# Performance work log

Hardware: AMD Instinct MI355X
Metric: run time of the kernel (lower is better)

The kernel has to match this reference:

```python
import jax, jax.numpy as jnp
import numpy as np

N = 100_000          # nodes
E = 1_600_000        # real edges (self-loops appended after)
HID = 32             # hidden_dim
RES = 5              # PersistenceImager resolution -> 5x5 image
SIGMA = 0.2          # gaussian bandwidth of persistence image kernel
PRELU_A = 0.1        # F.prelu weight used in the source


def _linear_init(k, fan_in, fan_out):
    k1, k2 = jax.random.split(k)
    s = 1.0 / np.sqrt(fan_in)
    W = jax.random.uniform(k1, (fan_in, fan_out), minval=-s, maxval=s, dtype=jnp.float32)
    b = jax.random.uniform(k2, (fan_out,), minval=-s, maxval=s, dtype=jnp.float32)
    return W, b


def setup_inputs() -> dict:
    key = jax.random.key(0)
    ks = jax.random.split(key, 10)
    # edge list: E random edges, then N self-loops appended at the END
    src = jax.random.randint(ks[0], (E,), 0, N)
    dst = jax.random.randint(ks[1], (E,), 0, N)
    loops = jnp.arange(N)
    edge_index0 = jnp.stack([jnp.concatenate([src, loops]),
                             jnp.concatenate([dst, loops])]).astype(jnp.int64)
    x0 = jax.random.normal(ks[2], (N, 1), dtype=jnp.float32)
    # GIN conv MLPs (Base_Model with out_dim=hidden_dim)
    W1, b1 = _linear_init(ks[3], 1, HID)
    W2, b2 = _linear_init(ks[4], HID, HID)
    W4, b4 = _linear_init(ks[5], HID, HID)
    W3, b3 = _linear_init(ks[6], HID, HID)   # conv3: Linear only, no ReLU
    W5, b5 = _linear_init(ks[7], 2 * HID, HID)  # lin5
    W6, b6 = _linear_init(ks[8], HID, 2)        # lin6
    return dict(x0=x0, edge_index0=edge_index0,
                W1=W1, b1=b1, W2=W2, b2=b2, W4=W4, b4=b4, W3=W3, b3=b3,
                W5=W5, b5=b5, W6=W6, b6=b6)


def _gin_agg(x, src, dst):
    # PyG GINConv with eps=0: (1+eps)*x + sum_{j->i} x_j  (aggregation over the
    # provided edge_index, which here already includes appended self-loops)
    return x + jax.ops.segment_sum(x[src], dst, num_segments=N)


def _prelu(x):
    return jnp.where(x >= 0, x, PRELU_A * x)


def _pers_image(pd):
    # Persistence image on a RESxRES grid over [0,1]^2 of (birth, persistence),
    # gaussian kernel integrated per pixel via normal CDFs, linear pers weight.
    b = pd[:, 0]
    pers = pd[:, 1] - pd[:, 0]
    edges = jnp.linspace(0.0, 1.0, RES + 1)
    inv = 1.0 / (SIGMA * np.sqrt(2.0))
    cdf_b = 0.5 * (1.0 + jax.lax.erf((edges[None, :] - b[:, None]) * inv))   # [E, RES+1]
    cdf_p = 0.5 * (1.0 + jax.lax.erf((edges[None, :] - pers[:, None]) * inv))
    db = cdf_b[:, 1:] - cdf_b[:, :-1]   # [E, RES]
    dp = cdf_p[:, 1:] - cdf_p[:, :-1]
    img = jnp.einsum('e,ei,ej->ij', pers, db, dp)
    return img.reshape(-1)  # [25]


def reference(x0, edge_index0, W1, b1, W2, b2, W4, b4, W3, b3, W5, b5, W6, b6):
    src, dst = edge_index0[0], edge_index0[1]
    # Base_Model GIN path (dropout is identity in eval mode); order 1,2,4,3
    x = jax.nn.relu(_gin_agg(x0, src, dst) @ W1 + b1)
    x = jax.nn.relu(_gin_agg(x, src, dst) @ W2 + b2)
    x = jax.nn.relu(_gin_agg(x, src, dst) @ W4 + b4)
    x = _gin_agg(x, src, dst) @ W3 + b3      # conv3: Linear, no ReLU
    # edge head over the E real edges (drop trailing N self-loops)
    x_in = x[src[:E]]
    x_out = x[dst[:E]]
    h = _prelu(jnp.concatenate([x_in, x_out], axis=-1) @ W5 + b5)
    pd = h @ W6 + b6                          # predicted PD, [E, 2]
    img = _pers_image(pd)                     # persistence image, [25]
    return pd, img
```

## Files before the change

### kernel.cpp

```cpp
#include <hip/hip_runtime.h>
#include <hip/hip_bf16.h>
#include <hip/hip_fp16.h>
#include <math.h>

#define NN 100000
#define EE 1600000
#define ET 1700000
#define HID 32

#define BKT_SHIFT 10
#define BKT_MASK 1023
#define NBKT 98
#define EPB 4096
#define NBLK_A 416

__global__ __launch_bounds__(128) void k_zero(int* __restrict__ p, int n) {
    int t = blockIdx.x * 128 + threadIdx.x;
    if (t < n) p[t] = 0;
}

__global__ __launch_bounds__(256) void k_bkt_count(const int* __restrict__ dst32, int* __restrict__ bucket_cnt) {
    __shared__ int h[NBKT];
    for (int i = threadIdx.x; i < NBKT; i += 256) h[i] = 0;
    __syncthreads();
    int base = blockIdx.x * EPB;
    for (int k = 0; k < EPB; k += 256) {
        int t = base + k + threadIdx.x;
        if (t < ET) atomicAdd(&h[dst32[t] >> BKT_SHIFT], 1);
    }
    __syncthreads();
    for (int i = threadIdx.x; i < NBKT; i += 256) {
        int c = h[i];
        if (c) atomicAdd(&bucket_cnt[i], c);
    }
}

__global__ __launch_bounds__(128) void k_bkt_scan(const int* __restrict__ bucket_cnt, int* __restrict__ bucket_base,
                                                  int* __restrict__ bucket_fill) {
    __shared__ int s[128];
    int t = threadIdx.x;
    int v = (t < NBKT) ? bucket_cnt[t] : 0;
    s[t] = v;
    for (int off = 1; off < 128; off <<= 1) {
        __syncthreads();
        int u = (t >= off) ? s[t - off] : 0;
        __syncthreads();
        s[t] += u;
    }
    __syncthreads();
    int ex = s[t] - v;
    if (t < NBKT) {
        bucket_base[t] = ex;
        bucket_fill[t] = ex;
    }
    if (t == 0) bucket_base[NBKT] = ET;
}

__global__ __launch_bounds__(256) void k_bkt_scatter(const int* __restrict__ src32, const int* __restrict__ dst32,
                                                     int* __restrict__ bucket_fill, int2* __restrict__ pairs) {
    __shared__ int h[NBKT];
    __shared__ int bbase[NBKT];
    for (int i = threadIdx.x; i < NBKT; i += 256) h[i] = 0;
    __syncthreads();
    int base = blockIdx.x * EPB;
    for (int k = 0; k < EPB; k += 256) {
        int t = base + k + threadIdx.x;
        if (t < ET) atomicAdd(&h[dst32[t] >> BKT_SHIFT], 1);
    }
    __syncthreads();
    for (int i = threadIdx.x; i < NBKT; i += 256) {
        int c = h[i];
        bbase[i] = c ? atomicAdd(&bucket_fill[i], c) : 0;
        h[i] = 0;
    }
    __syncthreads();
    for (int k = 0; k < EPB; k += 256) {
        int t = base + k + threadIdx.x;
        if (t < ET) {
            int sv = src32[t], dv = dst32[t];
            int b = dv >> BKT_SHIFT;
            int off = atomicAdd(&h[b], 1);
            pairs[bbase[b] + off] = make_int2(sv, dv);
        }
    }
}

__global__ __launch_bounds__(512) void k_bkt_csr(const int2* __restrict__ pairs, const int* __restrict__ bucket_base,
                                                 int* __restrict__ rowptr, int* __restrict__ src_sorted) {
    __shared__ int h[1024];
    __shared__ int tmp[512];
    int t = threadIdx.x;
    int b = blockIdx.x;
    int e0 = bucket_base[b], e1 = bucket_base[b + 1];
    int node0 = b << BKT_SHIFT;

    h[t] = 0;
    h[t + 512] = 0;
    __syncthreads();
    for (int e = e0 + t; e < e1; e += 512) atomicAdd(&h[pairs[e].y & BKT_MASK], 1);
    __syncthreads();

    int i0 = 2 * t, i1 = 2 * t + 1;
    int v0 = h[i0], v1 = h[i1];
    int s = v0 + v1;
    tmp[t] = s;
    for (int off = 1; off < 512; off <<= 1) {
        __syncthreads();
        int u = (t >= off) ? tmp[t - off] : 0;
        __syncthreads();
        tmp[t] += u;
    }
    __syncthreads();
    int excl = tmp[t] - s;
    h[i0] = excl;
    h[i1] = excl + v0;
    __syncthreads();

    for (int i = t; i < 1024; i += 512) {
        int node = node0 + i;
        if (node < NN) rowptr[node] = e0 + h[i];
    }
    if (b == 0 && t == 0) rowptr[NN] = ET;
    __syncthreads();

    for (int e = e0 + t; e < e1; e += 512) {
        int2 p = pairs[e];
        int sl = atomicAdd(&h[p.y & BKT_MASK], 1);
        src_sorted[e0 + sl] = p.x;
    }
}

__device__ __forceinline__ void acc4(uint2 r, float& c0, float& c1, float& c2, float& c3) {
    __half2 h0 = *reinterpret_cast<__half2*>(&r.x);
    __half2 h1 = *reinterpret_cast<__half2*>(&r.y);
    float2 f0 = __half22float2(h0);
    float2 f1 = __half22float2(h1);
    c0 += f0.x; c1 += f0.y; c2 += f1.x; c3 += f1.y;
}

__global__ __launch_bounds__(256) void k_pull1a(const int* __restrict__ rowptr, const int* __restrict__ src_sorted,
                                                const float* __restrict__ x0, float* __restrict__ agg0) {
    int g = blockIdx.x * 256 + threadIdx.x;
    if (g >= NN) return;
    int e0 = rowptr[g], e1 = rowptr[g + 1];
    float a0 = x0[g], a1 = 0.f, a2 = 0.f, a3 = 0.f, a4 = 0.f, a5 = 0.f, a6 = 0.f, a7 = 0.f;
    int e = e0;
    for (; e + 8 <= e1; e += 8) {
        a0 += x0[src_sorted[e + 0]];
        a1 += x0[src_sorted[e + 1]];
        a2 += x0[src_sorted[e + 2]];
        a3 += x0[src_sorted[e + 3]];
        a4 += x0[src_sorted[e + 4]];
        a5 += x0[src_sorted[e + 5]];
        a6 += x0[src_sorted[e + 6]];
        a7 += x0[src_sorted[e + 7]];
    }
    for (; e < e1; ++e) a0 += x0[src_sorted[e]];
    agg0[g] = ((a0 + a1) + (a2 + a3)) + ((a4 + a5) + (a6 + a7));
}

__global__ __launch_bounds__(256) void k_pull1b(const float* __restrict__ agg0, const float* __restrict__ W1,
                                                const float* __restrict__ b1, __half* __restrict__ hout) {
    int t = blockIdx.x * 256 + threadIdx.x;
    int g = t >> 3, j = t & 7;
    float s = agg0[g];
    float o0 = fmaxf(fmaf(s, W1[4 * j + 0], b1[4 * j + 0]), 0.f);
    float o1 = fmaxf(fmaf(s, W1[4 * j + 1], b1[4 * j + 1]), 0.f);
    float o2 = fmaxf(fmaf(s, W1[4 * j + 2], b1[4 * j + 2]), 0.f);
    float o3 = fmaxf(fmaf(s, W1[4 * j + 3], b1[4 * j + 3]), 0.f);
    __half2 p0 = __floats2half2_rn(o0, o1);
    __half2 p1 = __floats2half2_rn(o2, o3);
    uint2 st = make_uint2(*reinterpret_cast<unsigned*>(&p0), *reinterpret_cast<unsigned*>(&p1));
    reinterpret_cast<uint2*>(hout)[(g << 3) + j] = st;
}

template <int RELU>
__global__ __launch_bounds__(256) void k_agg_mm(const int* __restrict__ rowptr, const int* __restrict__ src_sorted,
                                                const __half* __restrict__ hin, const float* __restrict__ W,
                                                const float* __restrict__ b, __half* __restrict__ hout) {
    __shared__ float Wl[1024];
    for (int i = threadIdx.x; i < 1024; i += 256) Wl[i] = W[i];
    __syncthreads();
    int g = (blockIdx.x * 256 + threadIdx.x) >> 3;
    int j = threadIdx.x & 7;
    const uint2* tab = reinterpret_cast<const uint2*>(hin);
    int e0 = rowptr[g], e1 = rowptr[g + 1];
    float x0, x1, x2, x3;
    {
        uint2 r = tab[(g << 3) + j];
        __half2 h0 = *reinterpret_cast<__half2*>(&r.x);
        __half2 h1 = *reinterpret_cast<__half2*>(&r.y);
        float2 f0 = __half22float2(h0), f1 = __half22float2(h1);
        x0 = f0.x; x1 = f0.y; x2 = f1.x; x3 = f1.y;
    }
    float y0 = 0.f, y1 = 0.f, y2 = 0.f, y3 = 0.f;
    int e = e0;
    for (; e + 8 <= e1; e += 8) {
        int s0 = src_sorted[e + 0], s1 = src_sorted[e + 1], s2 = src_sorted[e + 2], s3 = src_sorted[e + 3];
        int s4 = src_sorted[e + 4], s5 = src_sorted[e + 5], s6 = src_sorted[e + 6], s7 = src_sorted[e + 7];
        uint2 r0 = tab[(s0 << 3) + j];
        uint2 r1 = tab[(s1 << 3) + j];
        uint2 r2 = tab[(s2 << 3) + j];
        uint2 r3 = tab[(s3 << 3) + j];
        uint2 r4 = tab[(s4 << 3) + j];
        uint2 r5 = tab[(s5 << 3) + j];
        uint2 r6 = tab[(s6 << 3) + j];
        uint2 r7 = tab[(s7 << 3) + j];
        acc4(r0, x0, x1, x2, x3);
        acc4(r1, y0, y1, y2, y3);
        acc4(r2, x0, x1, x2, x3);
        acc4(r3, y0, y1, y2, y3);
        acc4(r4, x0, x1, x2, x3);
        acc4(r5, y0, y1, y2, y3);
        acc4(r6, x0, x1, x2, x3);
        acc4(r7, y0, y1, y2, y3);
    }
    for (; e < e1; ++e) {
        uint2 r = tab[(src_sorted[e] << 3) + j];
        acc4(r, x0, x1, x2, x3);
    }
    x0 += y0; x1 += y1; x2 += y2; x3 += y3;

    float o0 = b[4 * j + 0], o1 = b[4 * j + 1], o2 = b[4 * j + 2], o3 = b[4 * j + 3];
#pragma unroll
    for (int k = 0; k < 8; ++k) {
        float f0 = __shfl(x0, k, 8);
        float f1 = __shfl(x1, k, 8);
        float f2 = __shfl(x2, k, 8);
        float f3 = __shfl(x3, k, 8);
        float4 w0 = *reinterpret_cast<const float4*>(&Wl[(4 * k + 0) * 32 + 4 * j]);
        float4 w1 = *reinterpret_cast<const float4*>(&Wl[(4 * k + 1) * 32 + 4 * j]);
        float4 w2 = *reinterpret_cast<const float4*>(&Wl[(4 * k + 2) * 32 + 4 * j]);
        float4 w3 = *reinterpret_cast<const float4*>(&Wl[(4 * k + 3) * 32 + 4 * j]);
        o0 = fmaf(f0, w0.x, o0); o1 = fmaf(f0, w0.y, o1); o2 = fmaf(f0, w0.z, o2); o3 = fmaf(f0, w0.w, o3);
        o0 = fmaf(f1, w1.x, o0); o1 = fmaf(f1, w1.y, o1); o2 = fmaf(f1, w1.z, o2); o3 = fmaf(f1, w1.w, o3);
        o0 = fmaf(f2, w2.x, o0); o1 = fmaf(f2, w2.y, o1); o2 = fmaf(f2, w2.z, o2); o3 = fmaf(f2, w2.w, o3);
        o0 = fmaf(f3, w3.x, o0); o1 = fmaf(f3, w3.y, o1); o2 = fmaf(f3, w3.z, o2); o3 = fmaf(f3, w3.w, o3);
    }
    if (RELU) {
        o0 = fmaxf(o0, 0.f); o1 = fmaxf(o1, 0.f); o2 = fmaxf(o2, 0.f); o3 = fmaxf(o3, 0.f);
    }
    __half2 p0 = __floats2half2_rn(o0, o1);
    __half2 p1 = __floats2half2_rn(o2, o3);
    uint2 st = make_uint2(*reinterpret_cast<unsigned*>(&p0), *reinterpret_cast<unsigned*>(&p1));
    reinterpret_cast<uint2*>(hout)[(g << 3) + j] = st;
}

__global__ __launch_bounds__(256) void k_agg_mm_proj(const int* __restrict__ rowptr, const int* __restrict__ src_sorted,
                                                     const __half* __restrict__ hin, const float* __restrict__ W3,
                                                     const float* __restrict__ b3,
                                                     const float* __restrict__ W5, const float* __restrict__ b5,
                                                     __half* __restrict__ u16, __half* __restrict__ v16) {
    __shared__ float W3l[1024];
    __shared__ float W5l[2048];
    for (int i = threadIdx.x; i < 1024; i += 256) W3l[i] = W3[i];
    for (int i = threadIdx.x; i < 2048; i += 256) W5l[i] = W5[i];
    __syncthreads();
    int g = (blockIdx.x * 256 + threadIdx.x) >> 3;
    int j = threadIdx.x & 7;
    const uint2* tab = reinterpret_cast<const uint2*>(hin);
    int e0 = rowptr[g], e1 = rowptr[g + 1];
    float x0, x1, x2, x3;
    {
        uint2 r = tab[(g << 3) + j];
        __half2 h0 = *reinterpret_cast<__half2*>(&r.x);
        __half2 h1 = *reinterpret_cast<__half2*>(&r.y);
        float2 f0 = __half22float2(h0), f1 = __half22float2(h1);
        x0 = f0.x; x1 = f0.y; x2 = f1.x; x3 = f1.y;
    }
    float y0 = 0.f, y1 = 0.f, y2 = 0.f, y3 = 0.f;
    int e = e0;
    for (; e + 8 <= e1; e += 8) {
        int s0 = src_sorted[e + 0], s1 = src_sorted[e + 1], s2 = src_sorted[e + 2], s3 = src_sorted[e + 3];
        int s4 = src_sorted[e + 4], s5 = src_sorted[e + 5], s6 = src_sorted[e + 6], s7 = src_sorted[e + 7];
        uint2 r0 = tab[(s0 << 3) + j];
        uint2 r1 = tab[(s1 << 3) + j];
        uint2 r2 = tab[(s2 << 3) + j];
        uint2 r3 = tab[(s3 << 3) + j];
        uint2 r4 = tab[(s4 << 3) + j];
        uint2 r5 = tab[(s5 << 3) + j];
        uint2 r6 = tab[(s6 << 3) + j];
        uint2 r7 = tab[(s7 << 3) + j];
        acc4(r0, x0, x1, x2, x3);
        acc4(r1, y0, y1, y2, y3);
        acc4(r2, x0, x1, x2, x3);
        acc4(r3, y0, y1, y2, y3);
        acc4(r4, x0, x1, x2, x3);
        acc4(r5, y0, y1, y2, y3);
        acc4(r6, x0, x1, x2, x3);
        acc4(r7, y0, y1, y2, y3);
    }
    for (; e < e1; ++e) {
        uint2 r = tab[(src_sorted[e] << 3) + j];
        acc4(r, x0, x1, x2, x3);
    }
    x0 += y0; x1 += y1; x2 += y2; x3 += y3;

    float o0 = b3[4 * j + 0], o1 = b3[4 * j + 1], o2 = b3[4 * j + 2], o3 = b3[4 * j + 3];
#pragma unroll
    for (int k = 0; k < 8; ++k) {
        float f0 = __shfl(x0, k, 8);
        float f1 = __shfl(x1, k, 8);
        float f2 = __shfl(x2, k, 8);
        float f3 = __shfl(x3, k, 8);
        float4 w0 = *reinterpret_cast<const float4*>(&W3l[(4 * k + 0) * 32 + 4 * j]);
        float4 w1 = *reinterpret_cast<const float4*>(&W3l[(4 * k + 1) * 32 + 4 * j]);
        float4 w2 = *reinterpret_cast<const float4*>(&W3l[(4 * k + 2) * 32 + 4 * j]);
        float4 w3 = *reinterpret_cast<const float4*>(&W3l[(4 * k + 3) * 32 + 4 * j]);
        o0 = fmaf(f0, w0.x, o0); o1 = fmaf(f0, w0.y, o1); o2 = fmaf(f0, w0.z, o2); o3 = fmaf(f0, w0.w, o3);
        o0 = fmaf(f1, w1.x, o0); o1 = fmaf(f1, w1.y, o1); o2 = fmaf(f1, w1.z, o2); o3 = fmaf(f1, w1.w, o3);
        o0 = fmaf(f2, w2.x, o0); o1 = fmaf(f2, w2.y, o1); o2 = fmaf(f2, w2.z, o2); o3 = fmaf(f2, w2.w, o3);
        o0 = fmaf(f3, w3.x, o0); o1 = fmaf(f3, w3.y, o1); o2 = fmaf(f3, w3.z, o2); o3 = fmaf(f3, w3.w, o3);
    }
    float u0 = b5[4 * j + 0], u1 = b5[4 * j + 1], u2 = b5[4 * j + 2], u3 = b5[4 * j + 3];
    float v0 = 0.f, v1 = 0.f, v2 = 0.f, v3 = 0.f;
#pragma unroll
    for (int k = 0; k < 8; ++k) {
        float f0 = __shfl(o0, k, 8);
        float f1 = __shfl(o1, k, 8);
        float f2 = __shfl(o2, k, 8);
        float f3 = __shfl(o3, k, 8);
        float4 a0 = *reinterpret_cast<const float4*>(&W5l[(4 * k + 0) * 32 + 4 * j]);
        float4 a1 = *reinterpret_cast<const float4*>(&W5l[(4 * k + 1) * 32 + 4 * j]);
        float4 a2 = *reinterpret_cast<const float4*>(&W5l[(4 * k + 2) * 32 + 4 * j]);
        float4 a3 = *reinterpret_cast<const float4*>(&W5l[(4 * k + 3) * 32 + 4 * j]);
        u0 = fmaf(f0, a0.x, u0); u1 = fmaf(f0, a0.y, u1); u2 = fmaf(f0, a0.z, u2); u3 = fmaf(f0, a0.w, u3);
        u0 = fmaf(f1, a1.x, u0); u1 = fmaf(f1, a1.y, u1); u2 = fmaf(f1, a1.z, u2); u3 = fmaf(f1, a1.w, u3);
        u0 = fmaf(f2, a2.x, u0); u1 = fmaf(f2, a2.y, u1); u2 = fmaf(f2, a2.z, u2); u3 = fmaf(f2, a2.w, u3);
        u0 = fmaf(f3, a3.x, u0); u1 = fmaf(f3, a3.y, u1); u2 = fmaf(f3, a3.z, u2); u3 = fmaf(f3, a3.w, u3);
        float4 c0 = *reinterpret_cast<const float4*>(&W5l[(32 + 4 * k + 0) * 32 + 4 * j]);
        float4 c1 = *reinterpret_cast<const float4*>(&W5l[(32 + 4 * k + 1) * 32 + 4 * j]);
        float4 c2 = *reinterpret_cast<const float4*>(&W5l[(32 + 4 * k + 2) * 32 + 4 * j]);
        float4 c3 = *reinterpret_cast<const float4*>(&W5l[(32 + 4 * k + 3) * 32 + 4 * j]);
        v0 = fmaf(f0, c0.x, v0); v1 = fmaf(f0, c0.y, v1); v2 = fmaf(f0, c0.z, v2); v3 = fmaf(f0, c0.w, v3);
        v0 = fmaf(f1, c1.x, v0); v1 = fmaf(f1, c1.y, v1); v2 = fmaf(f1, c1.z, v2); v3 = fmaf(f1, c1.w, v3);
        v0 = fmaf(f2, c2.x, v0); v1 = fmaf(f2, c2.y, v1); v2 = fmaf(f2, c2.z, v2); v3 = fmaf(f2, c2.w, v3);
        v0 = fmaf(f3, c3.x, v0); v1 = fmaf(f3, c3.y, v1); v2 = fmaf(f3, c3.z, v2); v3 = fmaf(f3, c3.w, v3);
    }
    __half2 pu0 = __floats2half2_rn(u0, u1);
    __half2 pu1 = __floats2half2_rn(u2, u3);
    uint2 su = make_uint2(*reinterpret_cast<unsigned*>(&pu0), *reinterpret_cast<unsigned*>(&pu1));
    reinterpret_cast<uint2*>(u16)[(g << 3) + j] = su;
    __half2 pv0 = __floats2half2_rn(v0, v1);
    __half2 pv1 = __floats2half2_rn(v2, v3);
    uint2 sv = make_uint2(*reinterpret_cast<unsigned*>(&pv0), *reinterpret_cast<unsigned*>(&pv1));
    reinterpret_cast<uint2*>(v16)[(g << 3) + j] = sv;
}

__device__ __forceinline__ void edge_pd(const uint4* pu, const uint4* pv, const float* W6,
                                        float b60, float b61, float& pd0, float& pd1) {
    pd0 = b60; pd1 = b61;
#pragma unroll
    for (int q = 0; q < 4; ++q) {
        uint4 ua = pu[q];
        uint4 vb = pv[q];
        const __half2* ah = reinterpret_cast<const __half2*>(&ua);
        const __half2* bh = reinterpret_cast<const __half2*>(&vb);
#pragma unroll
        for (int r = 0; r < 4; ++r) {
            float2 f = __half22float2(__hadd2(ah[r], bh[r]));
            int jj = q * 8 + 2 * r;
            float h0 = f.x >= 0.f ? f.x : 0.1f * f.x;
            float h1 = f.y >= 0.f ? f.y : 0.1f * f.y;
            pd0 = fmaf(h0, W6[2 * jj + 0], pd0);
            pd1 = fmaf(h0, W6[2 * jj + 1], pd1);
            pd0 = fmaf(h1, W6[2 * (jj + 1) + 0], pd0);
            pd1 = fmaf(h1, W6[2 * (jj + 1) + 1], pd1);
        }
    }
}

__global__ __launch_bounds__(256) void k_edge(const int* __restrict__ src32, const int* __restrict__ dst32,
                                              const __half* __restrict__ u16, const __half* __restrict__ v16,
                                              const float* __restrict__ W6, const float* __restrict__ b6,
                                              float* __restrict__ pd_out, float* __restrict__ partial) {
    int ea = blockIdx.x * 512 + threadIdx.x;
    int eb = ea + 256;
    int sa = src32[ea], da = dst32[ea];
    int sb = src32[eb], db = dst32[eb];
    const uint4* pua = reinterpret_cast<const uint4*>(u16 + ((size_t)sa << 5));
    const uint4* pva = reinterpret_cast<const uint4*>(v16 + ((size_t)da << 5));
    const uint4* pub = reinterpret_cast<const uint4*>(u16 + ((size_t)sb << 5));
    const uint4* pvb = reinterpret_cast<const uint4*>(v16 + ((size_t)db << 5));
    float b60 = b6[0], b61 = b6[1];

    float pda0, pda1, pdb0, pdb1;
    edge_pd(pua, pva, W6, b60, b61, pda0, pda1);
    edge_pd(pub, pvb, W6, b60, b61, pdb0, pdb1);
    reinterpret_cast<float2*>(pd_out)[ea] = make_float2(pda0, pda1);
    reinterpret_cast<float2*>(pd_out)[eb] = make_float2(pdb0, pdb1);

    float persA = pda1 - pda0;
    float persB = pdb1 - pdb0;
    const float inv = 3.5355339059327378f;
    float cbA[6], cpA[6], cbB[6], cpB[6];
#pragma unroll
    for (int i = 0; i < 6; ++i) {
        float te = 0.2f * (float)i;
        cbA[i] = 0.5f * (1.f + erff((te - pda0) * inv));
        cpA[i] = 0.5f * (1.f + erff((te - persA) * inv));
        cbB[i] = 0.5f * (1.f + erff((te - pdb0) * inv));
        cpB[i] = 0.5f * (1.f + erff((te - persB) * inv));
    }

    int lane = threadIdx.x & 63;
    int wv = threadIdx.x >> 6;
    __shared__ float sacc[4][25];
#pragma unroll
    for (int i = 0; i < 5; ++i) {
#pragma unroll
        for (int jj = 0; jj < 5; ++jj) {
            float v = persA * (cbA[i + 1] - cbA[i]) * (cpA[jj + 1] - cpA[jj])
                    + persB * (cbB[i + 1] - cbB[i]) * (cpB[jj + 1] - cpB[jj]);
            v += __shfl_down(v, 32);
            v += __shfl_down(v, 16);
            v += __shfl_down(v, 8);
            v += __shfl_down(v, 4);
            v += __shfl_down(v, 2);
            v += __shfl_down(v, 1);
            if (lane == 0) sacc[wv][i * 5 + jj] = v;
        }
    }
    __syncthreads();
    if (threadIdx.x < 25) {
        partial[(size_t)blockIdx.x * 25 + threadIdx.x] =
            sacc[0][threadIdx.x] + sacc[1][threadIdx.x] + sacc[2][threadIdx.x] + sacc[3][threadIdx.x];
    }
}

__global__ __launch_bounds__(256) void k_img(const float* __restrict__ partial, float* __restrict__ img) {
    int bin = blockIdx.x;
    float s = 0.f;
    for (int k = threadIdx.x; k < EE / 512; k += 256) s += partial[(size_t)k * 25 + bin];
    s += __shfl_down(s, 32);
    s += __shfl_down(s, 16);
    s += __shfl_down(s, 8);
    s += __shfl_down(s, 4);
    s += __shfl_down(s, 2);
    s += __shfl_down(s, 1);
    __shared__ float wsum[4];
    if ((threadIdx.x & 63) == 0) wsum[threadIdx.x >> 6] = s;
    __syncthreads();
    if (threadIdx.x == 0) img[bin] = wsum[0] + wsum[1] + wsum[2] + wsum[3];
}

extern "C" void kernel_launch(void* const* d_in, const int* in_sizes, int n_in,
                              void* d_out, int out_size, void* d_ws, size_t ws_size,
                              hipStream_t stream) {
    const float* x0 = (const float*)d_in[0];
    const int* src32 = (const int*)d_in[1];
    const int* dst32 = src32 + ET;
    const float* W1 = (const float*)d_in[2];
    const float* b1 = (const float*)d_in[3];
    const float* W2 = (const float*)d_in[4];
    const float* b2 = (const float*)d_in[5];
    const float* W4 = (const float*)d_in[6];
    const float* b4 = (const float*)d_in[7];
    const float* W3 = (const float*)d_in[8];
    const float* b3 = (const float*)d_in[9];
    const float* W5 = (const float*)d_in[10];
    const float* b5 = (const float*)d_in[11];
    const float* W6 = (const float*)d_in[12];
    const float* b6 = (const float*)d_in[13];
    float* out = (float*)d_out;

    char* w = (char*)d_ws;
    int2* pairs = (int2*)w;
    int* bucket_cnt = (int*)(pairs + ET);
    int* bucket_base = bucket_cnt + NBKT;
    int* bucket_fill = bucket_base + NBKT + 1;
    int* rowptr = bucket_fill + NBKT;
    int* src_sorted = rowptr + NN + 1;
    size_t off = ((size_t)((char*)(src_sorted + ET) - w) + 63) & ~(size_t)63;
    __half* bufA = (__half*)(w + off);
    __half* bufB = bufA + (size_t)NN * 32;
    __half* u16 = bufB + (size_t)NN * 32;
    __half* v16 = u16 + (size_t)NN * 32;
    float* agg0 = (float*)(v16 + (size_t)NN * 32);
    float* partial = agg0 + NN;

    k_zero<<<1, 128, 0, stream>>>(bucket_cnt, NBKT);
    k_bkt_count<<<NBLK_A, 256, 0, stream>>>(dst32, bucket_cnt);
    k_bkt_scan<<<1, 128, 0, stream>>>(bucket_cnt, bucket_base, bucket_fill);
    k_bkt_scatter<<<NBLK_A, 256, 0, stream>>>(src32, dst32, bucket_fill, pairs);
    k_bkt_csr<<<NBKT, 512, 0, stream>>>(pairs, bucket_base, rowptr, src_sorted);

    k_pull1a<<<(NN + 255) / 256, 256, 0, stream>>>(rowptr, src_sorted, x0, agg0);
    k_pull1b<<<NN * 8 / 256, 256, 0, stream>>>(agg0, W1, b1, bufA);
    k_agg_mm<1><<<NN * 8 / 256, 256, 0, stream>>>(rowptr, src_sorted, bufA, W2, b2, bufB);
    k_agg_mm<1><<<NN * 8 / 256, 256, 0, stream>>>(rowptr, src_sorted, bufB, W4, b4, bufA);
    k_agg_mm_proj<<<NN * 8 / 256, 256, 0, stream>>>(rowptr, src_sorted, bufA, W3, b3, W5, b5, u16, v16);

    k_edge<<<EE / 512, 256, 0, stream>>>(src32, dst32, u16, v16, W6, b6, out, partial);
    k_img<<<25, 256, 0, stream>>>(partial, out + 2 * (size_t)EE);
}
```

Baseline: 254.3 us.

## Process edges in dst-bucketed order with grid-stride loop and register image accumulation

The bucket scatter now also records each edge's original id. The edge head then walks the dst-bucketed pair list, so gathers of v16 rows hit nearby nodes and get better cache locality. Each thread accumulates the 25 image bins in registers across a grid-stride loop and reduces once per block, instead of doing a wave reduction for every pair of edges. It also folds the 0.5 CDF constants into a single 0.25 factor. The costs are scattered pd writes indexed by the original edge id, an extra index array written in the scatter, a self-loop filter branch, and higher register pressure from the 25 accumulators.

```diff
diff --git a/kernel.cpp b/kernel.cpp
--- a/kernel.cpp
+++ b/kernel.cpp
@@ -13,6 +13,7 @@
 #define NBKT 98
 #define EPB 4096
 #define NBLK_A 416
+#define NBE 1024
 
 __global__ __launch_bounds__(128) void k_zero(int* __restrict__ p, int n) {
     int t = blockIdx.x * 128 + threadIdx.x;
@@ -57,7 +58,8 @@
 }
 
 __global__ __launch_bounds__(256) void k_bkt_scatter(const int* __restrict__ src32, const int* __restrict__ dst32,
-                                                     int* __restrict__ bucket_fill, int2* __restrict__ pairs) {
+                                                     int* __restrict__ bucket_fill, int2* __restrict__ pairs,
+                                                     int* __restrict__ eidA) {
     __shared__ int h[NBKT];
     __shared__ int bbase[NBKT];
     for (int i = threadIdx.x; i < NBKT; i += 256) h[i] = 0;
@@ -80,7 +82,9 @@
             int sv = src32[t], dv = dst32[t];
             int b = dv >> BKT_SHIFT;
             int off = atomicAdd(&h[b], 1);
-            pairs[bbase[b] + off] = make_int2(sv, dv);
+            int slot = bbase[b] + off;
+            pairs[slot] = make_int2(sv, dv);
+            eidA[slot] = t;
         }
     }
 }
@@ -347,79 +351,76 @@
     reinterpret_cast<uint2*>(v16)[(g << 3) + j] = sv;
 }
 
-__device__ __forceinline__ void edge_pd(const uint4* pu, const uint4* pv, const float* W6,
-                                        float b60, float b61, float& pd0, float& pd1) {
-    pd0 = b60; pd1 = b61;
-#pragma unroll
-    for (int q = 0; q < 4; ++q) {
-        uint4 ua = pu[q];
-        uint4 vb = pv[q];
-        const __half2* ah = reinterpret_cast<const __half2*>(&ua);
-        const __half2* bh = reinterpret_cast<const __half2*>(&vb);
-#pragma unroll
-        for (int r = 0; r < 4; ++r) {
-            float2 f = __half22float2(__hadd2(ah[r], bh[r]));
-            int jj = q * 8 + 2 * r;
-            float h0 = f.x >= 0.f ? f.x : 0.1f * f.x;
-            float h1 = f.y >= 0.f ? f.y : 0.1f * f.y;
-            pd0 = fmaf(h0, W6[2 * jj + 0], pd0);
-            pd1 = fmaf(h0, W6[2 * jj + 1], pd1);
-            pd0 = fmaf(h1, W6[2 * (jj + 1) + 0], pd0);
-            pd1 = fmaf(h1, W6[2 * (jj + 1) + 1], pd1);
+__global__ __launch_bounds__(256) void k_edge2(const int2* __restrict__ pairs, const int* __restrict__ eidA,
+                                               const __half* __restrict__ u16, const __half* __restrict__ v16,
+                                               const float* __restrict__ W6, const float* __restrict__ b6,
+                                               float* __restrict__ pd_out, float* __restrict__ partial) {
+    float acc[25];
+#pragma unroll
+    for (int i = 0; i < 25; ++i) acc[i] = 0.f;
+    float b60 = b6[0], b61 = b6[1];
+    const float inv = 3.5355339059327378f;
+
+    int t0 = blockIdx.x * 256 + threadIdx.x;
+    const int stride = NBE * 256;
+    for (int e = t0; e < ET; e += stride) {
+        int2 p = pairs[e];
+        int eid = eidA[e];
+        if (eid < EE) {
+            const uint4* pu = reinterpret_cast<const uint4*>(u16 + ((size_t)p.x << 5));
+            const uint4* pv = reinterpret_cast<const uint4*>(v16 + ((size_t)p.y << 5));
+            float pd0 = b60, pd1 = b61;
+#pragma unroll
+            for (int q = 0; q < 4; ++q) {
+                uint4 ua = pu[q];
+                uint4 vb = pv[q];
+                const __half2* ah = reinterpret_cast<const __half2*>(&ua);
+                const __half2* bh = reinterpret_cast<const __half2*>(&vb);
+#pragma unroll
+                for (int r = 0; r < 4; ++r) {
+                    float2 f = __half22float2(__hadd2(ah[r], bh[r]));
+                    int jj = q * 8 + 2 * r;
+                    float h0 = f.x >= 0.f ? f.x : 0.1f * f.x;
+                    float h1 = f.y >= 0.f ? f.y : 0.1f * f.y;
+                    pd0 = fmaf(h0, W6[2 * jj + 0], pd0);
+                    pd1 = fmaf(h0, W6[2 * jj + 1], pd1);
+                    pd0 = fmaf(h1, W6[2 * (jj + 1) + 0], pd0);
+                    pd1 = fmaf(h1, W6[2 * (jj + 1) + 1], pd1);
+                }
+            }
+            reinterpret_cast<float2*>(pd_out)[eid] = make_float2(pd0, pd1);
+
+            float pers = pd1 - pd0;
+            float cb[6], cp[6];
+#pragma unroll
+            for (int i = 0; i < 6; ++i) {
+                float te = 0.2f * (float)i;
+                cb[i] = erff((te - pd0) * inv);
+                cp[i] = erff((te - pers) * inv);
+            }
+#pragma unroll
+            for (int i = 0; i < 5; ++i) {
+                float pdb = 0.25f * pers * (cb[i + 1] - cb[i]);
+#pragma unroll
+                for (int jj = 0; jj < 5; ++jj)
+                    acc[i * 5 + jj] = fmaf(pdb, cp[jj + 1] - cp[jj], acc[i * 5 + jj]);
+            }
         }
-    }
-}
-
-__global__ __launch_bounds__(256) void k_edge(const int* __restrict__ src32, const int* __restrict__ dst32,
-                                              const __half* __restrict__ u16, const __half* __restrict__ v16,
-                                              const float* __restrict__ W6, const float* __restrict__ b6,
-                                              float* __restrict__ pd_out, float* __restrict__ partial) {
-    int ea = blockIdx.x * 512 + threadIdx.x;
-    int eb = ea + 256;
-    int sa = src32[ea], da = dst32[ea];
-    int sb = src32[eb], db = dst32[eb];
-    const uint4* pua = reinterpret_cast<const uint4*>(u16 + ((size_t)sa << 5));
-    const uint4* pva = reinterpret_cast<const uint4*>(v16 + ((size_t)da << 5));
-    const uint4* pub = reinterpret_cast<const uint4*>(u16 + ((size_t)sb << 5));
-    const uint4* pvb = reinterpret_cast<const uint4*>(v16 + ((size_t)db << 5));
-    float b60 = b6[0], b61 = b6[1];
-
-    float pda0, pda1, pdb0, pdb1;
-    edge_pd(pua, pva, W6, b60, b61, pda0, pda1);
-    edge_pd(pub, pvb, W6, b60, b61, pdb0, pdb1);
-    reinterpret_cast<float2*>(pd_out)[ea] = make_float2(pda0, pda1);
-    reinterpret_cast<float2*>(pd_out)[eb] = make_float2(pdb0, pdb1);
-
-    float persA = pda1 - pda0;
-    float persB = pdb1 - pdb0;
-    const float inv = 3.5355339059327378f;
-    float cbA[6], cpA[6], cbB[6], cpB[6];
-#pragma unroll
-    for (int i = 0; i < 6; ++i) {
-        float te = 0.2f * (float)i;
-        cbA[i] = 0.5f * (1.f + erff((te - pda0) * inv));
-        cpA[i] = 0.5f * (1.f + erff((te - persA) * inv));
-        cbB[i] = 0.5f * (1.f + erff((te - pdb0) * inv));
-        cpB[i] = 0.5f * (1.f + erff((te - persB) * inv));
     }
 
     int lane = threadIdx.x & 63;
     int wv = threadIdx.x >> 6;
     __shared__ float sacc[4][25];
 #pragma unroll
-    for (int i = 0; i < 5; ++i) {
-#pragma unroll
-        for (int jj = 0; jj < 5; ++jj) {
-            float v = persA * (cbA[i + 1] - cbA[i]) * (cpA[jj + 1] - cpA[jj])
-                    + persB * (cbB[i + 1] - cbB[i]) * (cpB[jj + 1] - cpB[jj]);
-            v += __shfl_down(v, 32);
-            v += __shfl_down(v, 16);
-            v += __shfl_down(v, 8);
-            v += __shfl_down(v, 4);
-            v += __shfl_down(v, 2);
-            v += __shfl_down(v, 1);
-            if (lane == 0) sacc[wv][i * 5 + jj] = v;
-        }
+    for (int i = 0; i < 25; ++i) {
+        float v = acc[i];
+        v += __shfl_down(v, 32);
+        v += __shfl_down(v, 16);
+        v += __shfl_down(v, 8);
+        v += __shfl_down(v, 4);
+        v += __shfl_down(v, 2);
+        v += __shfl_down(v, 1);
+        if (lane == 0) sacc[wv][i] = v;
     }
     __syncthreads();
     if (threadIdx.x < 25) {
@@ -431,7 +432,7 @@
 __global__ __launch_bounds__(256) void k_img(const float* __restrict__ partial, float* __restrict__ img) {
     int bin = blockIdx.x;
     float s = 0.f;
-    for (int k = threadIdx.x; k < EE / 512; k += 256) s += partial[(size_t)k * 25 + bin];
+    for (int k = threadIdx.x; k < NBE; k += 256) s += partial[(size_t)k * 25 + bin];
     s += __shfl_down(s, 32);
     s += __shfl_down(s, 16);
     s += __shfl_down(s, 8);
@@ -466,7 +467,8 @@
 
     char* w = (char*)d_ws;
     int2* pairs = (int2*)w;
-    int* bucket_cnt = (int*)(pairs + ET);
+    int* eidA = (int*)(pairs + ET);
+    int* bucket_cnt = eidA + ET;
     int* bucket_base = bucket_cnt + NBKT;
     int* bucket_fill = bucket_base + NBKT + 1;
     int* rowptr = bucket_fill + NBKT;
@@ -482,7 +484,7 @@
     k_zero<<<1, 128, 0, stream>>>(bucket_cnt, NBKT);
     k_bkt_count<<<NBLK_A, 256, 0, stream>>>(dst32, bucket_cnt);
     k_bkt_scan<<<1, 128, 0, stream>>>(bucket_cnt, bucket_base, bucket_fill);
-    k_bkt_scatter<<<NBLK_A, 256, 0, stream>>>(src32, dst32, bucket_fill, pairs);
+    k_bkt_scatter<<<NBLK_A, 256, 0, stream>>>(src32, dst32, bucket_fill, pairs, eidA);
     k_bkt_csr<<<NBKT, 512, 0, stream>>>(pairs, bucket_base, rowptr, src_sorted);
 
     k_pull1a<<<(NN + 255) / 256, 256, 0, stream>>>(rowptr, src_sorted, x0, agg0);
@@ -491,6 +493,6 @@
     k_agg_mm<1><<<NN * 8 / 256, 256, 0, stream>>>(rowptr, src_sorted, bufB, W4, b4, bufA);
     k_agg_mm_proj<<<NN * 8 / 256, 256, 0, stream>>>(rowptr, src_sorted, bufA, W3, b3, W5, b5, u16, v16);
 
-    k_edge<<<EE / 512, 256, 0, stream>>>(src32, dst32, u16, v16, W6, b6, out, partial);
+    k_edge2<<<NBE, 256, 0, stream>>>(pairs, eidA, u16, v16, W6, b6, out, partial);
     k_img<<<25, 256, 0, stream>>>(partial, out + 2 * (size_t)EE);
 }
```

Result: no change. 259.1 us (+1.9%).
